# Performance work log

Hardware: AMD Instinct MI355X
Metric: run time of the kernel (lower is better)

The kernel has to match this reference:

```python
import jax, jax.numpy as jnp
import numpy as np

B, S, H, M, STEPS = 8, 1024, 1024, 4, 5
LN_EPS = 1e-5


def _gelu(x):
    return jax.nn.gelu(x, approximate=False)  # torch nn.GELU default is exact erf


def _layernorm(x, g, b):
    mu = jnp.mean(x, axis=-1, keepdims=True)
    var = jnp.mean((x - mu) ** 2, axis=-1, keepdims=True)
    return (x - mu) * jax.lax.rsqrt(var + LN_EPS) * g + b


def setup_inputs() -> dict:
    key = jax.random.key(0)
    ks = jax.random.split(key, 16)
    def w(k, shape, scale=0.02):
        return (jax.random.normal(k, shape) * scale).astype(jnp.float32)
    z = lambda *shape: jnp.zeros(shape, jnp.float32)
    o = lambda *shape: jnp.ones(shape, jnp.float32)
    return {
        "deterministic_state": jax.random.normal(ks[0], (B, S, H), jnp.float32),
        "superposition_state": jax.random.normal(ks[1], (B, S, H * M), jnp.float32),
        "context": jax.random.normal(ks[2], (B, H), jnp.float32),
        # reasoning_mode_selector: Linear(H,H) -> GELU -> Linear(H,2) -> Softmax
        "Wm1": w(ks[3], (H, H)), "bm1": z(H), "Wm2": w(ks[4], (H, 2)), "bm2": z(2),
        # reasoning_depth_controller: Linear(H,H//2) -> GELU -> Linear(H//2,STEPS) -> Softmax
        "Wd1": w(ks[5], (H, H // 2)), "bd1": z(H // 2), "Wd2": w(ks[6], (H // 2, STEPS)), "bd2": z(STEPS),
        # explicit_reasoning_steps (stacked over STEPS): Linear(2H,H)->GELU->Linear(H,H)->LayerNorm
        "We1": w(ks[7], (STEPS, 2 * H, H)), "be1": z(STEPS, H),
        "We2": w(ks[8], (STEPS, H, H)), "be2": z(STEPS, H),
        "ln_g": o(STEPS, H), "ln_b": z(STEPS, H),
        # reasoning_memory GRUCell(H,H); gate order r,z,n as in torch
        "W_ih": w(ks[9], (H, 3 * H)), "W_hh": w(ks[10], (H, 3 * H)),
        "b_ih": z(3 * H), "b_hh": z(3 * H),
        # implicit_reasoning: Linear(H*M,2H)->GELU->Linear(2H,H*M)->LayerNorm
        "Wi1": w(ks[11], (H * M, 2 * H)), "bi1": z(2 * H),
        "Wi2": w(ks[12], (2 * H, H * M)), "bi2": z(H * M),
        "lni_g": o(H * M), "lni_b": z(H * M),
    }


def _forward(deterministic_state, superposition_state, context,
             Wm1, bm1, Wm2, bm2, Wd1, bd1, Wd2, bd2,
             We1, be1, We2, be2, ln_g, ln_b,
             W_ih, W_hh, b_ih, b_hh,
             Wi1, bi1, Wi2, bi2, lni_g, lni_b):
    b, s, h = deterministic_state.shape
    # mode / depth selection from 2D context [B,H]
    mode_weights = jax.nn.softmax(_gelu(context @ Wm1 + bm1) @ Wm2 + bm2, axis=-1)   # [B,2]
    depth_weights = jax.nn.softmax(_gelu(context @ Wd1 + bd1) @ Wd2 + bd2, axis=-1)  # [B,STEPS]

    ctx_exp = jnp.broadcast_to(context[:, None, :], (b, s, h))  # context.unsqueeze(1).expand

    def gru_cell(x, hprev):  # x,hprev: [N,H]
        gi = x @ W_ih + b_ih
        gh = hprev @ W_hh + b_hh
        i_r, i_z, i_n = jnp.split(gi, 3, axis=-1)
        h_r, h_z, h_n = jnp.split(gh, 3, axis=-1)
        r = jax.nn.sigmoid(i_r + h_r)
        z = jax.nn.sigmoid(i_z + h_z)
        n = jnp.tanh(i_n + r * h_n)
        return (1.0 - z) * n + z * hprev

    def step(carry, params):
        state, memory = carry
        W1, b1, W2, b2, g, beta = params
        combined = jnp.concatenate([state, ctx_exp], axis=-1)          # [B,S,2H]
        next_state = _layernorm(_gelu(combined @ W1 + b1) @ W2 + b2, g, beta)
        mem = gru_cell(next_state.reshape(-1, h), memory.reshape(-1, h)).reshape(b, s, h)
        gated = next_state + 0.1 * mem
        return (gated, mem), gated

    init = (deterministic_state, jnp.zeros_like(deterministic_state))
    _, gated_states = jax.lax.scan(step, init, (We1, be1, We2, be2, ln_g, ln_b))  # [STEPS,B,S,H]
    explicit_result = jnp.einsum('bi,ibsh->bsh', depth_weights, gated_states)

    implicit_result = _layernorm(_gelu(superposition_state @ Wi1 + bi1) @ Wi2 + bi2, lni_g, lni_b)  # [B,S,M*H]
    implicit_det = implicit_result.reshape(b, s, M, h).mean(axis=2)  # [B,S,H]

    result = (mode_weights[:, 0, None, None] * implicit_det
              + mode_weights[:, 1, None, None] * explicit_result)
    return result, mode_weights, depth_weights, explicit_result, implicit_result


def reference(deterministic_state, superposition_state, context,
              Wm1, bm1, Wm2, bm2, Wd1, bd1, Wd2, bd2,
              We1, be1, We2, be2, ln_g, ln_b,
              W_ih, W_hh, b_ih, b_hh,
              Wi1, bi1, Wi2, bi2, lni_g, lni_b):
    return _forward(deterministic_state, superposition_state, context,
                    Wm1, bm1, Wm2, bm2, Wd1, bd1, Wd2, bd2,
                    We1, be1, We2, be2, ln_g, ln_b,
                    W_ih, W_hh, b_ih, b_hh,
                    Wi1, bi1, Wi2, bi2, lni_g, lni_b)
```

## Files before the change

kernel.cpp:

```cpp
#include <hip/hip_runtime.h>
#include <hip/hip_bf16.h>
#include <math.h>


typedef unsigned short bf16_t;
typedef __attribute__((ext_vector_type(8))) short s8v;
typedef __attribute__((ext_vector_type(4))) float f4v;

typedef const __attribute__((address_space(1))) void* gas_ptr;
typedef __attribute__((address_space(3))) void* las_ptr;

#define DEVFN static __device__ __forceinline__

DEVFN bf16_t f2b(float f) {
    union { float f; unsigned u; } v; v.f = f;
    unsigned r = v.u + 0x7FFFu + ((v.u >> 16) & 1u);
    return (bf16_t)(r >> 16);
}
DEVFN float b2f(bf16_t b) {
    union { unsigned u; float f; } v; v.u = ((unsigned)b) << 16; return v.f;
}
DEVFN float geluf(float x) { return 0.5f * x * (1.0f + erff(x * 0.70710678118654752f)); }
DEVFN float sigmf(float x) { return 1.0f / (1.0f + expf(-x)); }

template <int N_> DEVFN void waitvm() {
    if constexpr (N_ == 7)  asm volatile("s_waitcnt vmcnt(7)"  ::: "memory");
    if constexpr (N_ == 9)  asm volatile("s_waitcnt vmcnt(9)"  ::: "memory");
    if constexpr (N_ == 10) asm volatile("s_waitcnt vmcnt(10)" ::: "memory");
    if constexpr (N_ == 12) asm volatile("s_waitcnt vmcnt(12)" ::: "memory");
    __builtin_amdgcn_sched_barrier(0);
}
DEVFN void lgkm0() {
    asm volatile("s_waitcnt lgkmcnt(0)" ::: "memory");
    __builtin_amdgcn_sched_barrier(0);
}

static const long OUT_RESULT = 0;
static const long OUT_MODE   = 8388608;
static const long OUT_DEPTH  = 8388624;
static const long OUT_EXPL   = 8388664;
static const long OUT_IMPL   = 16777272;

static const long SLAB = 8388608;

#define RD_A(mh, c_) { _Pragma("unroll") \
    for (int mf = 0; mf < MF / 2; ++mf) { \
        aR[mf][0] = *(const s8v*)(lds + (c_) * BUFB + aL + kof0 + ((mh) * (BM / 2) + mf * 16) * 128); \
        aR[mf][1] = *(const s8v*)(lds + (c_) * BUFB + aL + kof1 + ((mh) * (BM / 2) + mf * 16) * 128); } }

#define RD_B(nh, c_, dst) { _Pragma("unroll") \
    for (int nf = 0; nf < NF / 2; ++nf) { \
        dst[nf][0] = *(const s8v*)(lds + (c_) * BUFB + bL + kof0 + ((nh) * (BN / 2) + nf * 16) * 128); \
        dst[nf][1] = *(const s8v*)(lds + (c_) * BUFB + bL + kof1 + ((nh) * (BN / 2) + nf * 16) * 128); } }

#define MFMA_Q(mh, nh, bset) { __builtin_amdgcn_s_setprio(1); _Pragma("unroll") \
    for (int mf = 0; mf < MF / 2; ++mf) { _Pragma("unroll") \
      for (int nf = 0; nf < NF / 2; ++nf) { _Pragma("unroll") \
        for (int ks = 0; ks < 2; ++ks) { \
          acc[(mh) * (MF / 2) + mf][(nh) * (NF / 2) + nf] = \
            __builtin_amdgcn_mfma_f32_16x16x32_bf16(aR[mf][ks], bset[nf][ks], \
                acc[(mh) * (MF / 2) + mf][(nh) * (NF / 2) + nf], 0, 0, 0); } } } \
    __builtin_amdgcn_s_setprio(0); }

#define KTILE(c_, STG) {                                            \
    RD_A(0, c_); RD_B(0, c_, bR0);                                  \
    waitvm<V1>();                                                   \
    __builtin_amdgcn_s_barrier();                                   \
    lgkm0();                                                        \
    MFMA_Q(0, 0, bR0);                                              \
    __builtin_amdgcn_s_barrier();                                   \
    RD_B(1, c_, bR1);                                               \
    if (STG) { stgA(0, c_); stgB(0, c_); }                          \
    waitvm<V24>();                                                  \
    __builtin_amdgcn_s_barrier();                                   \
    lgkm0();                                                        \
    MFMA_Q(0, 1, bR1);                                              \
    __builtin_amdgcn_s_barrier();                                   \
    RD_A(1, c_);                                                    \
    if (STG) { stgB(1, c_); }                                       \
    __builtin_amdgcn_s_barrier();                                   \
    lgkm0();                                                        \
    MFMA_Q(1, 1, bR1);                                              \
    __builtin_amdgcn_s_barrier();                                   \
    if (STG) { stgA(1, c_); }                                       \
    waitvm<V24>();                                                  \
    __builtin_amdgcn_s_barrier();                                   \
    MFMA_Q(1, 0, bR0);                                              \
    __builtin_amdgcn_s_barrier();                                   \
}

template <int MF, int NF, int EPI>
__global__ __launch_bounds__(512, 2) void gemm8p(
    const bf16_t* __restrict__ A, const bf16_t* __restrict__ Bt,
    const float* __restrict__ bias, bf16_t* __restrict__ outB, int N, int K)
{
    constexpr int BM = MF * 32;
    constexpr int BN = NF * 64;
    constexpr int LA = BM / 64;
    constexpr int LB = BN / 64;
    constexpr int sA = LA / 2;
    constexpr int sB = LB / 2;
    constexpr int V1 = 3 * sA + 2 * sB;
    constexpr int V24 = 3 * (sA + sB);
    constexpr int ABYTES = BM * 128;
    constexpr int BUFB = (BM + BN) * 128;

    __shared__ __align__(16) char lds[2 * BUFB];

    const int tid  = threadIdx.x;
    const int lane = tid & 63;
    const int wave = tid >> 6;
    const int wm = wave >> 2, wn = wave & 3;
    const int l15 = lane & 15, lhi = lane >> 4, l7 = lane & 7;

    const int gx = gridDim.x;
    const int nwg = gx * gridDim.y;
    const int orig = blockIdx.y * gx + blockIdx.x;
    const int qq = nwg >> 3, rr8 = nwg & 7;
    const int xcd = orig & 7, lid = orig >> 3;
    const int nid = (xcd < rr8 ? xcd * (qq + 1) : rr8 * (qq + 1) + (xcd - rr8) * qq) + lid;
    const int m0 = (nid / gx) * BM;
    const int n0 = (nid % gx) * BN;

    const int NT = K >> 6;

    const int b2k = l7 >> 2;
    const int lx  = lhi ^ (l7 & 3);
    const unsigned aL   = (unsigned)((wm * (BM / 4) + l15) * 128 + (lx << 4));
    const unsigned bL   = (unsigned)(ABYTES + (wn * (BN / 8) + l15) * 128 + (lx << 4));
    const unsigned kof0 = (unsigned)(b2k << 6);
    const unsigned kof1 = (unsigned)((b2k ^ 1) << 6);

    f4v acc[MF][NF];
#pragma unroll
    for (int i = 0; i < MF; ++i)
#pragma unroll
        for (int j = 0; j < NF; ++j)
#pragma unroll
            for (int q2 = 0; q2 < 4; ++q2) acc[i][j][q2] = 0.0f;

    s8v aR[MF / 2][2];
    s8v bR0[NF / 2][2], bR1[NF / 2][2];

    const bf16_t* pA[LA];
    const bf16_t* pB[LB];
#pragma unroll
    for (int i = 0; i < LA; ++i) {
        const int li = i * 512 + tid;
        const int r = li >> 3, s = li & 7;
        pA[i] = A + (long)(m0 + r) * K + ((s ^ (r & 7)) << 3);
    }
#pragma unroll
    for (int i = 0; i < LB; ++i) {
        const int li = i * 512 + tid;
        const int r = li >> 3, s = li & 7;
        pB[i] = Bt + (long)(n0 + r) * K + ((s ^ (r & 7)) << 3);
    }

    auto stgA = [&](int h, int cbuf) {
#pragma unroll
        for (int i = 0; i < sA; ++i)
            __builtin_amdgcn_global_load_lds((gas_ptr)pA[h * sA + i],
                (las_ptr)(lds + cbuf * BUFB + (h * sA + i) * 8192 + tid * 16), 16, 0, 0);
    };
    auto stgB = [&](int h, int cbuf) {
#pragma unroll
        for (int i = 0; i < sB; ++i)
            __builtin_amdgcn_global_load_lds((gas_ptr)pB[h * sB + i],
                (las_ptr)(lds + cbuf * BUFB + ABYTES + (h * sB + i) * 8192 + tid * 16), 16, 0, 0);
    };
    auto adv = [&]() {
#pragma unroll
        for (int i = 0; i < LA; ++i) pA[i] += 64;
#pragma unroll
        for (int i = 0; i < LB; ++i) pB[i] += 64;
    };

    stgA(0, 0); stgB(0, 0); stgB(1, 0); stgA(1, 0); adv();
    stgA(0, 1); stgB(0, 1); stgB(1, 1); stgA(1, 1); adv();
    waitvm<V24>();
    __builtin_amdgcn_s_barrier();

    for (int t = 0; t < NT - 2; t += 2) {
        KTILE(0, true);  adv();
        KTILE(1, true);  adv();
    }
    asm volatile("s_waitcnt vmcnt(0)" ::: "memory");
    __builtin_amdgcn_sched_barrier(0);
    __builtin_amdgcn_s_barrier();
    KTILE(0, false);
    KTILE(1, false);

    const int crr = lhi << 2;
#pragma unroll
    for (int mh = 0; mh < 2; ++mh) {
#pragma unroll
        for (int mf = 0; mf < MF / 2; ++mf) {
#pragma unroll
            for (int nh = 0; nh < 2; ++nh) {
#pragma unroll
                for (int nf = 0; nf < NF / 2; ++nf) {
                    const int col = n0 + nh * (BN / 2) + wn * (BN / 8) + nf * 16 + l15;
#pragma unroll
                    for (int q2 = 0; q2 < 4; ++q2) {
                        const int row = m0 + mh * (BM / 2) + wm * (BM / 4) + mf * 16 + crr + q2;
                        const float v = acc[mh * (MF / 2) + mf][nh * (NF / 2) + nf][q2];
                        if (EPI == 1) {
                            outB[(long)row * N + col] = f2b(geluf(v + bias[col]));
                        } else if (EPI == 2) {
                            outB[(long)row * N + col] = f2b(geluf(v + bias[(long)(row >> 10) * N + col]));
                        } else {
                            outB[(long)row * N + col] = f2b(v + bias[col]);
                        }
                    }
                }
            }
        }
    }
}

__global__ __launch_bounds__(256) void transpose_k(
    const float* __restrict__ src, bf16_t* __restrict__ dst,
    int K, int N, long sbs, long dbs)
{
    __shared__ float tile[32][33];
    const float* s = src + (long)blockIdx.z * sbs;
    bf16_t* d = dst + (long)blockIdx.z * dbs;
    const int n0 = blockIdx.x * 32, k0 = blockIdx.y * 32;
    const int tx = threadIdx.x, ty = threadIdx.y;
#pragma unroll
    for (int i = 0; i < 4; ++i)
        tile[ty + i * 8][tx] = s[(long)(k0 + ty + i * 8) * N + n0 + tx];
    __syncthreads();
#pragma unroll
    for (int i = 0; i < 4; ++i)
        d[(long)(n0 + ty + i * 8) * K + k0 + tx] = f2b(tile[tx][ty + i * 8]);
}

__global__ __launch_bounds__(256) void cvt_k(const float4* __restrict__ src,
                                             ushort4* __restrict__ dst, int n4)
{
    const int i = blockIdx.x * 256 + threadIdx.x;
    if (i < n4) {
        float4 v = src[i];
        ushort4 o; o.x = f2b(v.x); o.y = f2b(v.y); o.z = f2b(v.z); o.w = f2b(v.w);
        dst[i] = o;
    }
}

__global__ __launch_bounds__(256) void colgemv8_k(
    const float* __restrict__ ctx, const float* __restrict__ Wbase, long wts,
    int Wld, const float* __restrict__ bias, long bts,
    float* __restrict__ out, long ots, int do_gelu)
{
    __shared__ float cs[8][1024];
    __shared__ float rr[16][16][8];
    const int j0 = blockIdx.x * 16;
    const int t = blockIdx.y;
    const int tid = threadIdx.x;
    for (int i = tid; i < 2048; i += 256)
        ((float4*)cs)[i] = ((const float4*)ctx)[i];
    __syncthreads();
    const int kp = tid >> 4, jj = tid & 15;
    const float* Wp = Wbase + (long)t * wts;
    float p[8] = {0, 0, 0, 0, 0, 0, 0, 0};
    for (int i = 0; i < 64; ++i) {
        const int k = kp * 64 + i;
        const float w = Wp[(long)k * Wld + j0 + jj];
#pragma unroll
        for (int b = 0; b < 8; ++b) p[b] = fmaf(cs[b][k], w, p[b]);
    }
#pragma unroll
    for (int b = 0; b < 8; ++b) rr[kp][jj][b] = p[b];
    __syncthreads();
    if (tid < 128) {
        const int jj2 = tid >> 3, b = tid & 7;
        float s = 0.f;
#pragma unroll
        for (int k2 = 0; k2 < 16; ++k2) s += rr[k2][jj2][b];
        s += bias[(long)t * bts + j0 + jj2];
        if (do_gelu) s = geluf(s);
        out[(long)t * ots + (long)b * Wld + j0 + jj2] = s;
    }
}

__global__ __launch_bounds__(256) void selB_k(
    const float* __restrict__ h1, const float* __restrict__ hd,
    const float* __restrict__ Wm2, const float* __restrict__ bm2,
    const float* __restrict__ Wd2, const float* __restrict__ bd2,
    float* __restrict__ outM, float* __restrict__ outD,
    float* __restrict__ wsM, float* __restrict__ wsD)
{
    const int b = blockIdx.x, tid = threadIdx.x;
    __shared__ float red[256];
    float lm[2], ld[5];
    for (int o = 0; o < 2; ++o) {
        float p = 0.f;
        for (int k = tid; k < 1024; k += 256) p += h1[b * 1024 + k] * Wm2[k * 2 + o];
        red[tid] = p; __syncthreads();
        for (int s = 128; s > 0; s >>= 1) { if (tid < s) red[tid] += red[tid + s]; __syncthreads(); }
        lm[o] = red[0] + bm2[o]; __syncthreads();
    }
    for (int o = 0; o < 5; ++o) {
        float p = 0.f;
        for (int k = tid; k < 512; k += 256) p += hd[b * 512 + k] * Wd2[k * 5 + o];
        red[tid] = p; __syncthreads();
        for (int s = 128; s > 0; s >>= 1) { if (tid < s) red[tid] += red[tid + s]; __syncthreads(); }
        ld[o] = red[0] + bd2[o]; __syncthreads();
    }
    if (tid == 0) {
        float mx = fmaxf(lm[0], lm[1]);
        float e0 = expf(lm[0] - mx), e1 = expf(lm[1] - mx);
        float inv = 1.f / (e0 + e1);
        outM[b * 2] = e0 * inv; outM[b * 2 + 1] = e1 * inv;
        wsM[b * 2] = e0 * inv;  wsM[b * 2 + 1] = e1 * inv;
        float md = ld[0];
        for (int o = 1; o < 5; ++o) md = fmaxf(md, ld[o]);
        float es[5]; float sum = 0.f;
        for (int o = 0; o < 5; ++o) { es[o] = expf(ld[o] - md); sum += es[o]; }
        for (int o = 0; o < 5; ++o) { outD[b * 5 + o] = es[o] / sum; wsD[b * 5 + o] = es[o] / sum; }
    }
}

__global__ __launch_bounds__(256) void ln1024_k(
    const bf16_t* __restrict__ X, const float* __restrict__ g,
    const float* __restrict__ b, bf16_t* __restrict__ Yb)
{
    const int row = blockIdx.x, tid = threadIdx.x;
    const ushort4 xv = ((const ushort4*)(X + (long)row * 1024))[tid];
    const float x0 = b2f(xv.x), x1 = b2f(xv.y), x2 = b2f(xv.z), x3 = b2f(xv.w);
    float s = x0 + x1 + x2 + x3;
    float ss = x0 * x0 + x1 * x1 + x2 * x2 + x3 * x3;
#pragma unroll
    for (int o = 32; o > 0; o >>= 1) { s += __shfl_down(s, o); ss += __shfl_down(ss, o); }
    __shared__ float rs[4], rss[4];
    const int wv = tid >> 6, ln = tid & 63;
    if (ln == 0) { rs[wv] = s; rss[wv] = ss; }
    __syncthreads();
    const float S = rs[0] + rs[1] + rs[2] + rs[3];
    const float SS = rss[0] + rss[1] + rss[2] + rss[3];
    const float mean = S * (1.0f / 1024.0f);
    const float var = SS * (1.0f / 1024.0f) - mean * mean;
    const float rstd = rsqrtf(var + 1e-5f);
    const float4 gv = ((const float4*)g)[tid];
    const float4 bv = ((const float4*)b)[tid];
    ushort4 ob;
    ob.x = f2b((x0 - mean) * rstd * gv.x + bv.x);
    ob.y = f2b((x1 - mean) * rstd * gv.y + bv.y);
    ob.z = f2b((x2 - mean) * rstd * gv.z + bv.z);
    ob.w = f2b((x3 - mean) * rstd * gv.w + bv.w);
    ((ushort4*)(Yb + (long)row * 1024))[tid] = ob;
}

template <bool FIRST>
__global__ __launch_bounds__(256) void gru_k(
    const bf16_t* __restrict__ gi, const bf16_t* __restrict__ gh,
    const float* __restrict__ bhh, const bf16_t* __restrict__ nsB,
    bf16_t* __restrict__ memB, bf16_t* __restrict__ stateOut)
{
    const long i4 = (long)blockIdx.x * 256 + threadIdx.x;
    const long row = i4 >> 8;
    const int h4 = (int)(i4 & 255) << 2;
    const bf16_t* gir = gi + row * 3072 + h4;
    const ushort4 vir = *(const ushort4*)(gir);
    const ushort4 viz = *(const ushort4*)(gir + 1024);
    const ushort4 vin = *(const ushort4*)(gir + 2048);
    float hr[4], hz[4], hn[4];
    if (FIRST) {
        const float4 a = *(const float4*)(bhh + h4);
        const float4 c = *(const float4*)(bhh + 1024 + h4);
        const float4 d = *(const float4*)(bhh + 2048 + h4);
        hr[0] = a.x; hr[1] = a.y; hr[2] = a.z; hr[3] = a.w;
        hz[0] = c.x; hz[1] = c.y; hz[2] = c.z; hz[3] = c.w;
        hn[0] = d.x; hn[1] = d.y; hn[2] = d.z; hn[3] = d.w;
    } else {
        const bf16_t* ghr = gh + row * 3072 + h4;
        const ushort4 g1 = *(const ushort4*)(ghr);
        const ushort4 g2 = *(const ushort4*)(ghr + 1024);
        const ushort4 g3 = *(const ushort4*)(ghr + 2048);
        hr[0] = b2f(g1.x); hr[1] = b2f(g1.y); hr[2] = b2f(g1.z); hr[3] = b2f(g1.w);
        hz[0] = b2f(g2.x); hz[1] = b2f(g2.y); hz[2] = b2f(g2.z); hz[3] = b2f(g2.w);
        hn[0] = b2f(g3.x); hn[1] = b2f(g3.y); hn[2] = b2f(g3.z); hn[3] = b2f(g3.w);
    }
    const ushort4 nsv = *(const ushort4*)(nsB + row * 1024 + h4);
    float mo[4] = {0.f, 0.f, 0.f, 0.f};
    if (!FIRST) {
        const ushort4 mv = *(const ushort4*)(memB + row * 1024 + h4);
        mo[0] = b2f(mv.x); mo[1] = b2f(mv.y); mo[2] = b2f(mv.z); mo[3] = b2f(mv.w);
    }
    const float ir[4] = {b2f(vir.x), b2f(vir.y), b2f(vir.z), b2f(vir.w)};
    const float iz[4] = {b2f(viz.x), b2f(viz.y), b2f(viz.z), b2f(viz.w)};
    const float in_[4] = {b2f(vin.x), b2f(vin.y), b2f(vin.z), b2f(vin.w)};
    const float ns[4] = {b2f(nsv.x), b2f(nsv.y), b2f(nsv.z), b2f(nsv.w)};
    ushort4 mnb, stb;
    float mn[4], gt[4];
#pragma unroll
    for (int i = 0; i < 4; ++i) {
        const float rg = sigmf(ir[i] + hr[i]);
        const float zg = sigmf(iz[i] + hz[i]);
        const float ng = tanhf(in_[i] + rg * hn[i]);
        mn[i] = (1.0f - zg) * ng + zg * mo[i];
        gt[i] = ns[i] + 0.1f * mn[i];
    }
    mnb.x = f2b(mn[0]); mnb.y = f2b(mn[1]); mnb.z = f2b(mn[2]); mnb.w = f2b(mn[3]);
    stb.x = f2b(gt[0]); stb.y = f2b(gt[1]); stb.z = f2b(gt[2]); stb.w = f2b(gt[3]);
    *(ushort4*)(memB + row * 1024 + h4) = mnb;
    *(ushort4*)(stateOut + row * 1024 + h4) = stb;
}

__global__ __launch_bounds__(1024) void ln4096_final_k(
    const bf16_t* __restrict__ Ypre, const float* __restrict__ g,
    const float* __restrict__ b, const bf16_t* __restrict__ stS,
    const float* __restrict__ depthw, float* __restrict__ implOut,
    float* __restrict__ explOut, float* __restrict__ result,
    const float* __restrict__ modew)
{
    const int row = blockIdx.x, tid = threadIdx.x;
    const ushort4 xv = ((const ushort4*)(Ypre + (long)row * 4096))[tid];
    const float x0 = b2f(xv.x), x1 = b2f(xv.y), x2 = b2f(xv.z), x3 = b2f(xv.w);
    float s = x0 + x1 + x2 + x3;
    float ss = x0 * x0 + x1 * x1 + x2 * x2 + x3 * x3;
#pragma unroll
    for (int o = 32; o > 0; o >>= 1) { s += __shfl_down(s, o); ss += __shfl_down(ss, o); }
    __shared__ float rs[16], rss[16];
    __shared__ float ylds[4096];
    const int wv = tid >> 6, ln = tid & 63;
    if (ln == 0) { rs[wv] = s; rss[wv] = ss; }
    __syncthreads();
    if (tid < 64) {
        float a = (ln < 16) ? rs[ln] : 0.f;
        float c2 = (ln < 16) ? rss[ln] : 0.f;
#pragma unroll
        for (int o = 8; o > 0; o >>= 1) { a += __shfl_down(a, o); c2 += __shfl_down(c2, o); }
        if (ln == 0) { rs[0] = a; rss[0] = c2; }
    }
    __syncthreads();
    const float mean = rs[0] * (1.f / 4096.f);
    const float var = rss[0] * (1.f / 4096.f) - mean * mean;
    const float rstd = rsqrtf(var + 1e-5f);
    const float4 gv = ((const float4*)g)[tid];
    const float4 bv = ((const float4*)b)[tid];
    float4 y;
    y.x = (x0 - mean) * rstd * gv.x + bv.x;
    y.y = (x1 - mean) * rstd * gv.y + bv.y;
    y.z = (x2 - mean) * rstd * gv.z + bv.z;
    y.w = (x3 - mean) * rstd * gv.w + bv.w;
    ((float4*)(implOut + (long)row * 4096))[tid] = y;
    ((float4*)ylds)[tid] = y;
    __syncthreads();
    const int bidx = row >> 10;
    const long off = (long)row * 1024 + tid;
    float ex = 0.f;
#pragma unroll
    for (int tt = 0; tt < 5; ++tt)
        ex += depthw[bidx * 5 + tt] * b2f(stS[(long)tt * SLAB + off]);
    explOut[off] = ex;
    const float det4 = 0.25f * (ylds[tid] + ylds[tid + 1024] + ylds[tid + 2048] + ylds[tid + 3072]);
    result[off] = modew[bidx * 2] * det4 + modew[bidx * 2 + 1] * ex;
}

extern "C" void kernel_launch(void* const* d_in, const int* in_sizes, int n_in,
                              void* d_out, int out_size, void* d_ws, size_t ws_size,
                              hipStream_t stream)
{
    const float* det    = (const float*)d_in[0];
    const float* super_ = (const float*)d_in[1];
    const float* ctx    = (const float*)d_in[2];
    const float* Wm1 = (const float*)d_in[3];
    const float* bm1 = (const float*)d_in[4];
    const float* Wm2 = (const float*)d_in[5];
    const float* bm2 = (const float*)d_in[6];
    const float* Wd1 = (const float*)d_in[7];
    const float* bd1 = (const float*)d_in[8];
    const float* Wd2 = (const float*)d_in[9];
    const float* bd2 = (const float*)d_in[10];
    const float* We1 = (const float*)d_in[11];
    const float* be1 = (const float*)d_in[12];
    const float* We2 = (const float*)d_in[13];
    const float* be2 = (const float*)d_in[14];
    const float* ln_g = (const float*)d_in[15];
    const float* ln_b = (const float*)d_in[16];
    const float* W_ih = (const float*)d_in[17];
    const float* W_hh = (const float*)d_in[18];
    const float* b_ih = (const float*)d_in[19];
    const float* b_hh = (const float*)d_in[20];
    const float* Wi1 = (const float*)d_in[21];
    const float* bi1 = (const float*)d_in[22];
    const float* Wi2 = (const float*)d_in[23];
    const float* bi2 = (const float*)d_in[24];
    const float* lni_g = (const float*)d_in[25];
    const float* lni_b = (const float*)d_in[26];

    float* out = (float*)d_out;
    char* W = (char*)d_ws;

    bf16_t* We1sT = (bf16_t*)(W + 0);
    bf16_t* We2T  = (bf16_t*)(W + 10485760L);
    bf16_t* WihT  = (bf16_t*)(W + 20971520L);
    bf16_t* WhhT  = (bf16_t*)(W + 27262976L);
    bf16_t* Wi1T  = (bf16_t*)(W + 33554432L);
    bf16_t* Wi2T  = (bf16_t*)(W + 50331648L);
    float* ctxbias = (float*)(W + 67108864L);
    float* modew   = (float*)(W + 67272704L);
    float* depthw  = (float*)(W + 67272768L);
    float* h1ws    = (float*)(W + 67276800L);
    float* hdws    = (float*)(W + 67309568L);
    const long SB = 67325952L;
    bf16_t* stateS = (bf16_t*)(W + SB);
    bf16_t* Zb     = (bf16_t*)(W + SB + 100663296L);
    bf16_t* memb   = (bf16_t*)(W + SB + 117440512L);
    bf16_t* nsB    = (bf16_t*)(W + SB + 134217728L);
    bf16_t* gi     = (bf16_t*)(W + SB + 150994944L);
    bf16_t* gh     = (bf16_t*)(W + SB + 201326592L);
    bf16_t* Y1     = gi;
    bf16_t* superb = gi;
    bf16_t* Yi     = (bf16_t*)(W + SB + 201326592L + 16777216L);
    bf16_t* Ypre   = gi;

    (void)in_sizes; (void)n_in; (void)out_size; (void)ws_size;

    dim3 tb(32, 8);

    colgemv8_k<<<dim3(64, 1), 256, 0, stream>>>(ctx, Wm1, 0, 1024, bm1, 0, h1ws, 0, 1);
    colgemv8_k<<<dim3(32, 1), 256, 0, stream>>>(ctx, Wd1, 0, 512, bd1, 0, hdws, 0, 1);
    colgemv8_k<<<dim3(64, 5), 256, 0, stream>>>(ctx, We1 + 1048576L, 2097152L, 1024,
                                                be1, 1024, ctxbias, 8192, 0);
    selB_k<<<8, 256, 0, stream>>>(h1ws, hdws, Wm2, bm2, Wd2, bd2,
                                  out + OUT_MODE, out + OUT_DEPTH, modew, depthw);

    transpose_k<<<dim3(32, 32, 5), tb, 0, stream>>>(We1, We1sT, 1024, 1024, 2097152L, 1048576L);
    transpose_k<<<dim3(32, 32, 5), tb, 0, stream>>>(We2, We2T, 1024, 1024, 1048576L, 1048576L);
    transpose_k<<<dim3(96, 32, 1), tb, 0, stream>>>(W_ih, WihT, 1024, 3072, 0L, 0L);
    transpose_k<<<dim3(96, 32, 1), tb, 0, stream>>>(W_hh, WhhT, 1024, 3072, 0L, 0L);
    transpose_k<<<dim3(64, 128, 1), tb, 0, stream>>>(Wi1, Wi1T, 4096, 2048, 0L, 0L);
    transpose_k<<<dim3(128, 64, 1), tb, 0, stream>>>(Wi2, Wi2T, 2048, 4096, 0L, 0L);

    cvt_k<<<8192, 256, 0, stream>>>((const float4*)det, (ushort4*)stateS, 2097152);

    for (int t = 0; t < 5; ++t) {
        const bf16_t* stIn = stateS + (long)t * SLAB;
        bf16_t* stOut = stateS + (long)(t + 1) * SLAB;
        gemm8p<4, 4, 2><<<dim3(4, 64), 512, 0, stream>>>(stIn, We1sT + (long)t * 1048576,
                                                         ctxbias + (long)t * 8192, Y1, 1024, 1024);
        gemm8p<4, 4, 3><<<dim3(4, 64), 512, 0, stream>>>(Y1, We2T + (long)t * 1048576,
                                                         be2 + t * 1024, Zb, 1024, 1024);
        ln1024_k<<<8192, 256, 0, stream>>>(Zb, ln_g + t * 1024, ln_b + t * 1024, nsB);
        gemm8p<4, 4, 3><<<dim3(12, 64), 512, 0, stream>>>(nsB, WihT, b_ih, gi, 3072, 1024);
        if (t > 0)
            gemm8p<4, 4, 3><<<dim3(12, 64), 512, 0, stream>>>(memb, WhhT, b_hh, gh, 3072, 1024);
        if (t == 0)
            gru_k<true><<<8192, 256, 0, stream>>>(gi, gh, b_hh, nsB, memb, stOut);
        else
            gru_k<false><<<8192, 256, 0, stream>>>(gi, gh, b_hh, nsB, memb, stOut);
    }

    cvt_k<<<32768, 256, 0, stream>>>((const float4*)super_, (ushort4*)superb, 8388608);
    gemm8p<8, 4, 1><<<dim3(8, 32), 512, 0, stream>>>(superb, Wi1T, bi1, Yi, 2048, 4096);
    gemm8p<8, 4, 3><<<dim3(16, 32), 512, 0, stream>>>(Yi, Wi2T, bi2, Ypre, 4096, 2048);
    ln4096_final_k<<<8192, 1024, 0, stream>>>(Ypre, lni_g, lni_b, stateS + SLAB, depthw,
                                              out + OUT_IMPL, out + OUT_EXPL,
                                              out + OUT_RESULT, modew);
}
```

Baseline: 1.477 ms.

## Software-pipeline LDS fragment reads across k-tiles in 8-wave GEMM

Restructures the GEMM k-loop so the LDS-to-register reads for the next k-tile (A half 0, both B halves) are issued right after the final MFMA quarter of the current tile, and are prefetched before the loop. It also removes the explicit lgkmcnt(0) waits and several barriers, and retunes the vmcnt wait thresholds. The aim is to hide LDS read latency behind MFMA work and cut synchronisation stalls. The risk is a race between reading the other buffer and the global-to-LDS stages still writing it, plus higher register pressure from keeping more fragments live.

```diff
diff --git a/kernel.cpp b/kernel.cpp
--- a/kernel.cpp
+++ b/kernel.cpp
@@ -24,14 +24,15 @@
 DEVFN float sigmf(float x) { return 1.0f / (1.0f + expf(-x)); }
 
 template <int N_> DEVFN void waitvm() {
-    if constexpr (N_ == 7)  asm volatile("s_waitcnt vmcnt(7)"  ::: "memory");
+    if constexpr (N_ == 0)  asm volatile("s_waitcnt vmcnt(0)"  ::: "memory");
+    if constexpr (N_ == 6)  asm volatile("s_waitcnt vmcnt(6)"  ::: "memory");
+    if constexpr (N_ == 8)  asm volatile("s_waitcnt vmcnt(8)"  ::: "memory");
     if constexpr (N_ == 9)  asm volatile("s_waitcnt vmcnt(9)"  ::: "memory");
-    if constexpr (N_ == 10) asm volatile("s_waitcnt vmcnt(10)" ::: "memory");
     if constexpr (N_ == 12) asm volatile("s_waitcnt vmcnt(12)" ::: "memory");
     __builtin_amdgcn_sched_barrier(0);
 }
-DEVFN void lgkm0() {
-    asm volatile("s_waitcnt lgkmcnt(0)" ::: "memory");
+DEVFN void barp() {
+    __builtin_amdgcn_s_barrier();
     __builtin_amdgcn_sched_barrier(0);
 }
 
@@ -63,30 +64,27 @@
     __builtin_amdgcn_s_setprio(0); }
 
 #define KTILE(c_, STG) {                                            \
-    RD_A(0, c_); RD_B(0, c_, bR0);                                  \
-    waitvm<V1>();                                                   \
-    __builtin_amdgcn_s_barrier();                                   \
-    lgkm0();                                                        \
+    __builtin_amdgcn_s_barrier();                         \
     MFMA_Q(0, 0, bR0);                                              \
-    __builtin_amdgcn_s_barrier();                                   \
-    RD_B(1, c_, bR1);                                               \
+    barp();                                               \
     if (STG) { stgA(0, c_); stgB(0, c_); }                          \
-    waitvm<V24>();                                                  \
-    __builtin_amdgcn_s_barrier();                                   \
-    lgkm0();                                                        \
+    waitvm<V2>();                                                   \
+    __builtin_amdgcn_s_barrier();                         \
     MFMA_Q(0, 1, bR1);                                              \
-    __builtin_amdgcn_s_barrier();                                   \
     RD_A(1, c_);                                                    \
+    barp();                                               \
     if (STG) { stgB(1, c_); }                                       \
-    __builtin_amdgcn_s_barrier();                                   \
-    lgkm0();                                                        \
+    waitvm<V3>();                                                   \
+    __builtin_amdgcn_s_barrier();                         \
     MFMA_Q(1, 1, bR1);                                              \
-    __builtin_amdgcn_s_barrier();                                   \
+    RD_B(1, (c_) ^ 1, bR1);                                         \
+    barp();                                               \
     if (STG) { stgA(1, c_); }                                       \
-    waitvm<V24>();                                                  \
-    __builtin_amdgcn_s_barrier();                                   \
+    waitvm<V2>();                                                   \
+    __builtin_amdgcn_s_barrier();                         \
     MFMA_Q(1, 0, bR0);                                              \
-    __builtin_amdgcn_s_barrier();                                   \
+    RD_A(0, (c_) ^ 1);                                              \
+    RD_B(0, (c_) ^ 1, bR0);                                         \
 }
 
 template <int MF, int NF, int EPI>
@@ -100,8 +98,8 @@
     constexpr int LB = BN / 64;
     constexpr int sA = LA / 2;
     constexpr int sB = LB / 2;
-    constexpr int V1 = 3 * sA + 2 * sB;
-    constexpr int V24 = 3 * (sA + sB);
+    constexpr int V2 = 3 * (sA + sB);
+    constexpr int V3 = 2 * (sA + sB);
     constexpr int ABYTES = BM * 128;
     constexpr int BUFB = (BM + BN) * 128;
 
@@ -178,16 +176,18 @@
 
     stgA(0, 0); stgB(0, 0); stgB(1, 0); stgA(1, 0); adv();
     stgA(0, 1); stgB(0, 1); stgB(1, 1); stgA(1, 1); adv();
-    waitvm<V24>();
+    waitvm<V3>();
     __builtin_amdgcn_s_barrier();
+    __builtin_amdgcn_sched_barrier(0);
+    RD_A(0, 0); RD_B(0, 0, bR0); RD_B(1, 0, bR1);
 
     for (int t = 0; t < NT - 2; t += 2) {
         KTILE(0, true);  adv();
         KTILE(1, true);  adv();
     }
-    asm volatile("s_waitcnt vmcnt(0)" ::: "memory");
+    waitvm<0>();
+    __builtin_amdgcn_s_barrier();
     __builtin_amdgcn_sched_barrier(0);
-    __builtin_amdgcn_s_barrier();
     KTILE(0, false);
     KTILE(1, false);
 
```

Result: no change. 1.492 ms (+1.0%).
